# Performance work log

Hardware: AMD Instinct MI355X
Metric: run time of the kernel (lower is better)

## Reference

```python
import jax, jax.numpy as jnp
import numpy as np

H = 12
D_MODEL = 768
H_D = D_MODEL // H


def setup_inputs() -> dict:
    key = jax.random.key(0)
    ks = jax.random.split(key, 11)
    B, S = 2, 2048
    scale_in = 1.0
    w_scale = 1.0 / np.sqrt(D_MODEL)
    inp = {
        "query": jax.random.normal(ks[0], (B, S, D_MODEL), dtype=jnp.float32),
        "key": jax.random.normal(ks[1], (B, S, D_MODEL), dtype=jnp.float32),
        "value": jax.random.normal(ks[2], (B, S, D_MODEL), dtype=jnp.float32),
        "wq": jax.random.normal(ks[3], (D_MODEL, D_MODEL), dtype=jnp.float32) * w_scale,
        "bq": jnp.zeros((D_MODEL,), dtype=jnp.float32),
        "wk": jax.random.normal(ks[4], (D_MODEL, D_MODEL), dtype=jnp.float32) * w_scale,
        "bk": jnp.zeros((D_MODEL,), dtype=jnp.float32),
        "wv": jax.random.normal(ks[5], (D_MODEL, D_MODEL), dtype=jnp.float32) * w_scale,
        "bv": jnp.zeros((D_MODEL,), dtype=jnp.float32),
        "wo": jax.random.normal(ks[6], (D_MODEL, D_MODEL), dtype=jnp.float32) * w_scale,
        "bo": jnp.zeros((D_MODEL,), dtype=jnp.float32),
    }
    return inp


def reference(query, key, value, wq, bq, wk, bk, wv, bv, wo, bo):
    B, S, _ = query.shape
    # QKV projections, split into heads: [B, H, S, h_d]
    def proj(x, w, b):
        y = jnp.einsum("bsd,de->bse", x, w) + b
        return y.reshape(B, S, H, H_D).transpose(0, 2, 1, 3)

    q = proj(query, wq, bq)
    k = proj(key, wk, bk)
    v = proj(value, wv, bv)

    # scaled dot-product attention (dropout disabled / eval mode)
    scores = jnp.einsum("bhsd,bhtd->bhst", q, k) / jnp.sqrt(jnp.float32(H_D))
    wm = jax.nn.softmax(scores, axis=-1)  # [B, H, S, S]
    out = jnp.einsum("bhst,bhtd->bhsd", wm, v)

    # merge heads and output projection
    out = out.transpose(0, 2, 1, 3).reshape(B, S, D_MODEL)
    out = jnp.einsum("bsd,de->bse", out, wo) + bo
    return out
```

## Files before the change

kernel.cpp:

```cpp
#include <hip/hip_runtime.h>

#define H 12
#define DM 768
#define HD 64
#define SEQ 2048
#define BATCH 2
#define MROWS (BATCH*SEQ)

typedef __attribute__((ext_vector_type(8))) short short8;
typedef __attribute__((ext_vector_type(4))) float f32x4;
typedef __attribute__((ext_vector_type(16))) float f32x16;
using u16 = unsigned short;
using u32 = unsigned int;

__device__ __forceinline__ float bf2f(u16 u) { return __uint_as_float(((u32)u) << 16); }
__device__ __forceinline__ u16 f2bf(float x) {
  u32 u = __float_as_uint(x);
  return (u16)((u + 0x7fffu + ((u >> 16) & 1u)) >> 16);
}
__device__ __forceinline__ u32 cvt_pk_bf16(float lo, float hi) {
  u32 r;
  asm("v_cvt_pk_bf16_f32 %0, %1, %2" : "=v"(r) : "v"(lo), "v"(hi));
  return r;
}
__device__ __forceinline__ float fexp2(float x) {
  float r;
  asm("v_exp_f32 %0, %1" : "=v"(r) : "v"(x));
  return r;
}
__device__ __forceinline__ void gl2lds16(const u16* __restrict__ g, u16* l) {
  __builtin_amdgcn_global_load_lds(
      (const __attribute__((address_space(1))) unsigned int*)g,
      (__attribute__((address_space(3))) unsigned int*)l,
      16, 0, 0);
}

#define C_SM 0.18033688011112042f

__global__ __launch_bounds__(256) void transpose_w4(const float* __restrict__ w0, const float* __restrict__ w1,
                                                    const float* __restrict__ w2, const float* __restrict__ w3,
                                                    u16* __restrict__ dst0)
{
  __shared__ u16 Ts[64][72];
  const float* src = blockIdx.z == 0 ? w0 : blockIdx.z == 1 ? w1 : blockIdx.z == 2 ? w2 : w3;
  u16* dst = dst0 + (size_t)blockIdx.z * DM * DM;
  const int t = threadIdx.x;
  const int r0 = blockIdx.y * 64, c0 = blockIdx.x * 64;
  const int row = t >> 2, cq = (t & 3) * 16;
  const float* sp = src + (size_t)(r0 + row) * DM + c0 + cq;
  #pragma unroll
  for (int g = 0; g < 4; ++g) {
    float4 a = *reinterpret_cast<const float4*>(sp + g * 4);
    Ts[row][cq + g * 4 + 0] = f2bf(a.x);
    Ts[row][cq + g * 4 + 1] = f2bf(a.y);
    Ts[row][cq + g * 4 + 2] = f2bf(a.z);
    Ts[row][cq + g * 4 + 3] = f2bf(a.w);
  }
  __syncthreads();
  union { uint4 v[2]; u16 e[16]; } pk;
  #pragma unroll
  for (int j = 0; j < 16; ++j) pk.e[j] = Ts[cq + j][row];
  uint4* dp = reinterpret_cast<uint4*>(dst + (size_t)(c0 + row) * DM + r0 + cq);
  dp[0] = pk.v[0];
  dp[1] = pk.v[1];
}

template<int BM, bool AF32>
__device__ __forceinline__ void gemm_core(const void* __restrict__ Av, const u16* __restrict__ Bt,
                                          const float* __restrict__ bias, void* __restrict__ dstv,
                                          int mode, int bx, int by, float outScale)
{
  constexpr int AFR = BM / 32;
  constexpr int ACH = BM / 32;
  __shared__ u16 As[BM * 64];
  __shared__ u16 Bs[128 * 64];
  const int t = threadIdx.x;
  const int lane = t & 63, w = t >> 6;
  const int l15 = lane & 15, l4 = lane >> 4;
  const int m0 = by * BM, n0 = bx * 128;
  const int wr = (w >> 1) * (BM / 2), wc = (w & 1) * 64;

  f32x4 acc[AFR][4] = {};

  for (int kt = 0; kt < DM / 64; ++kt) {
    const int k0 = kt * 64;
    #pragma unroll
    for (int c = 0; c < ACH; ++c) {
      const int id = c * 256 + t;
      const int row = id >> 3, xc = id & 7;
      const int db = row * 128 + ((xc * 16) ^ ((row & 7) << 4));
      if (AF32) {
        const float* Af = reinterpret_cast<const float*>(Av) + (size_t)(m0 + row) * DM + k0 + xc * 8;
        float4 a0 = *reinterpret_cast<const float4*>(Af);
        float4 a1 = *reinterpret_cast<const float4*>(Af + 4);
        uint4 v;
        v.x = cvt_pk_bf16(a0.x, a0.y);
        v.y = cvt_pk_bf16(a0.z, a0.w);
        v.z = cvt_pk_bf16(a1.x, a1.y);
        v.w = cvt_pk_bf16(a1.z, a1.w);
        *reinterpret_cast<uint4*>(reinterpret_cast<char*>(As) + db) = v;
      } else {
        uint4 va = *reinterpret_cast<const uint4*>(reinterpret_cast<const u16*>(Av) +
                   (size_t)(m0 + row) * DM + k0 + xc * 8);
        *reinterpret_cast<uint4*>(reinterpret_cast<char*>(As) + db) = va;
      }
    }
    #pragma unroll
    for (int c = 0; c < 4; ++c) {
      const int id = c * 256 + t;
      const int row = id >> 3, xc = id & 7;
      const int db = row * 128 + ((xc * 16) ^ ((row & 7) << 4));
      uint4 vb = *reinterpret_cast<const uint4*>(Bt + (size_t)(n0 + row) * DM + k0 + xc * 8);
      *reinterpret_cast<uint4*>(reinterpret_cast<char*>(Bs) + db) = vb;
    }
    __syncthreads();
    #pragma unroll
    for (int ks = 0; ks < 2; ++ks) {
      short8 ag[AFR], bg[4];
      #pragma unroll
      for (int i = 0; i < AFR; ++i) {
        const int ar = wr + i * 16 + l15;
        ag[i] = *reinterpret_cast<const short8*>(reinterpret_cast<const char*>(As) +
                 ar * 128 + ((ks * 64 + l4 * 16) ^ ((ar & 7) << 4)));
      }
      #pragma unroll
      for (int j = 0; j < 4; ++j) {
        const int br = wc + j * 16 + l15;
        bg[j] = *reinterpret_cast<const short8*>(reinterpret_cast<const char*>(Bs) +
                 br * 128 + ((ks * 64 + l4 * 16) ^ ((br & 7) << 4)));
      }
      #pragma unroll
      for (int i = 0; i < AFR; ++i)
        #pragma unroll
        for (int j = 0; j < 4; ++j)
          acc[i][j] = __builtin_amdgcn_mfma_f32_16x16x32_bf16(ag[i], bg[j], acc[i][j], 0, 0, 0);
    }
    __syncthreads();
  }

  #pragma unroll
  for (int j = 0; j < 4; ++j) {
    const int gcol = n0 + wc + j * 16 + l15;
    const float bb = bias[gcol];
    #pragma unroll
    for (int i = 0; i < AFR; ++i) {
      const int grow = m0 + wr + i * 16 + l4 * 4;
      if (mode == 2) {
        float* dst = reinterpret_cast<float*>(dstv);
        #pragma unroll
        for (int r = 0; r < 4; ++r)
          dst[(size_t)(grow + r) * DM + gcol] = acc[i][j][r] + bb;
      } else {
        u16* dst = reinterpret_cast<u16*>(dstv);
        const int b = grow >> 11, s = grow & (SEQ - 1);
        const int h = gcol >> 6, d = gcol & 63;
        if (mode == 0) {
          #pragma unroll
          for (int r = 0; r < 4; ++r)
            dst[((size_t)(b * H + h) * SEQ + s + r) * HD + d] = f2bf((acc[i][j][r] + bb) * outScale);
        } else {
          union { uint2 v; u16 e[4]; } pk;
          #pragma unroll
          for (int r = 0; r < 4; ++r) pk.e[r] = f2bf(acc[i][j][r] + bb);
          *reinterpret_cast<uint2*>(dst + ((size_t)(b * H + h) * HD + d) * SEQ + s) = pk.v;
        }
      }
    }
  }
}

__global__ __launch_bounds__(256) void gemm_qkv_kernel(
    const float* __restrict__ xq, const float* __restrict__ xk, const float* __restrict__ xv,
    const u16* __restrict__ wT, const float* __restrict__ bq, const float* __restrict__ bk,
    const float* __restrict__ bv, u16* __restrict__ Qb, u16* __restrict__ Kb, u16* __restrict__ Vtb)
{
  const int flat = blockIdx.z * 384 + blockIdx.y * 6 + blockIdx.x;
  const int nb = (flat & 7) * 144 + (flat >> 3);
  const int z = nb / 384, rem = nb % 384;
  const int by = rem / 6, bx = rem % 6;
  const float* A    = z == 0 ? xq : z == 1 ? xk : xv;
  const u16* Bt     = wT + (size_t)z * DM * DM;
  const float* bias = z == 0 ? bq : z == 1 ? bk : bv;
  u16* dst          = z == 0 ? Qb : z == 1 ? Kb : Vtb;
  const float sc    = z == 1 ? C_SM : 1.0f;
  gemm_core<64, true>(A, Bt, bias, dst, z == 2 ? 1 : 0, bx, by, sc);
}

__global__ __launch_bounds__(256) void gemm_o_kernel(const u16* __restrict__ A, const u16* __restrict__ woT,
                                                     const float* __restrict__ bo, float* __restrict__ out)
{
  const int flat = blockIdx.y * 6 + blockIdx.x;
  const int nb = (flat & 7) * 96 + (flat >> 3);
  gemm_core<32, false>(A, woT, bo, out, 2, nb % 6, nb / 6, 1.0f);
}

__global__ __launch_bounds__(256) void attn_kernel(const u16* __restrict__ Q, const u16* __restrict__ K,
                                                   const u16* __restrict__ Vt,
                                                   float* __restrict__ Op0, float* __restrict__ Op1,
                                                   float* __restrict__ Lp0, float* __restrict__ Lp1)
{
  __shared__ u16 Ks[3][64 * 64];
  __shared__ u16 Vs[3][64 * 64];
  const int t = threadIdx.x;
  const int lane = t & 63, w = t >> 6;
  const int l31 = lane & 31, hi = lane >> 5;
  const int flat = blockIdx.y * 32 + blockIdx.x;
  const int nbid = (flat & 7) * 96 + (flat >> 3);
  const int bh = nbid >> 5;
  const int rem = nbid & 31;
  const int q0 = (rem >> 1) * 128;
  const int half = rem & 1;
  const int kv0 = half * (SEQ / 2);
  const size_t qbase  = ((size_t)bh * SEQ + q0) * HD;
  const size_t kbase0 = (size_t)bh * SEQ * HD;
  const size_t vtbase = (size_t)bh * HD * SEQ;
  float* __restrict__ Op = half ? Op1 : Op0;
  float* __restrict__ Lp = half ? Lp1 : Lp0;
  constexpr int NT = SEQ / 2 / 64;

  const int r8 = lane >> 3;
  const int pcol = ((lane & 7) ^ r8) * 8;

  short8 qf[4];
  {
    const u16* qp = Q + qbase + (size_t)(w * 32 + l31) * HD + hi * 8;
    #pragma unroll
    for (int ks = 0; ks < 4; ++ks)
      qf[ks] = *reinterpret_cast<const short8*>(qp + ks * 16);
  }

  auto STAGE = [&](int pt, int buf) {
    #pragma unroll
    for (int j = 0; j < 2; ++j) {
      const int ci = w * 2 + j;
      const int row = ci * 8 + r8;
      gl2lds16(K + kbase0 + (size_t)(kv0 + pt * 64 + row) * HD + pcol, &Ks[buf][ci * 512]);
      gl2lds16(Vt + vtbase + (size_t)row * SEQ + kv0 + pt * 64 + pcol, &Vs[buf][ci * 512]);
    }
  };

  STAGE(0, 0);
  STAGE(1, 1);

  short8 ones;
  #pragma unroll
  for (int j = 0; j < 8; ++j) ones[j] = (short)0x3F80;

  f32x16 oacc[2] = {};
  f32x16 accL = {};
  int cur = 0;

  for (int kt = 0; kt < NT; ++kt) {
    asm volatile("s_waitcnt vmcnt(4)" ::: "memory");
    __builtin_amdgcn_s_barrier();

    {
      const int pt = (kt + 2) & (NT - 1);
      const int pbuf = (cur + 2) % 3;
      STAGE(pt, pbuf);
    }

    f32x16 s0 = {}, s1 = {};
    __builtin_amdgcn_s_setprio(1);
    #pragma unroll
    for (int ks = 0; ks < 4; ++ks) {
      const int cb = ks * 32 + hi * 16;
      short8 kf0 = *reinterpret_cast<const short8*>(reinterpret_cast<const char*>(Ks[cur]) +
                   l31 * 128 + (cb ^ ((l31 & 7) << 4)));
      short8 kf1 = *reinterpret_cast<const short8*>(reinterpret_cast<const char*>(Ks[cur]) +
                   (32 + l31) * 128 + (cb ^ ((l31 & 7) << 4)));
      s0 = __builtin_amdgcn_mfma_f32_32x32x16_bf16(kf0, qf[ks], s0, 0, 0, 0);
      s1 = __builtin_amdgcn_mfma_f32_32x32x16_bf16(kf1, qf[ks], s1, 0, 0, 0);
    }
    __builtin_amdgcn_s_setprio(0);

    float p0[16], p1[16];
    #pragma unroll
    for (int r = 0; r < 16; ++r) {
      p0[r] = fexp2(s0[r]);
      p1[r] = fexp2(s1[r]);
    }

    __builtin_amdgcn_s_setprio(1);
    #pragma unroll
    for (int ks2 = 0; ks2 < 4; ++ks2) {
      const float* P = (ks2 < 2) ? p0 : p1;
      const int ro = (ks2 & 1) * 8;
      u32 a0 = cvt_pk_bf16(P[ro + 0], P[ro + 1]);
      u32 a1 = cvt_pk_bf16(P[ro + 2], P[ro + 3]);
      u32 b0 = cvt_pk_bf16(P[ro + 4], P[ro + 5]);
      u32 b1 = cvt_pk_bf16(P[ro + 6], P[ro + 7]);
      asm volatile("v_permlane32_swap_b32 %0, %1" : "+v"(a0), "+v"(b0));
      asm volatile("v_permlane32_swap_b32 %0, %1" : "+v"(a1), "+v"(b1));
      union { u32 u[4]; short8 s; } pa;
      pa.u[0] = a0; pa.u[1] = a1; pa.u[2] = b0; pa.u[3] = b1;
      accL = __builtin_amdgcn_mfma_f32_32x32x16_bf16(pa.s, ones, accL, 0, 0, 0);
      #pragma unroll
      for (int dt = 0; dt < 2; ++dt) {
        const int vr = dt * 32 + l31;
        short8 vf = *reinterpret_cast<const short8*>(reinterpret_cast<const char*>(Vs[cur]) +
                    vr * 128 + ((ks2 * 32 + hi * 16) ^ ((vr & 7) << 4)));
        oacc[dt] = __builtin_amdgcn_mfma_f32_32x32x16_bf16(pa.s, vf, oacc[dt], 0, 0, 0);
      }
    }
    __builtin_amdgcn_s_setprio(0);
    cur = (cur == 2) ? 0 : cur + 1;
  }

  if (l31 == 0) {
    #pragma unroll
    for (int r = 0; r < 16; ++r) {
      const int qo = (r & 3) + 8 * (r >> 2) + 4 * hi;
      Lp[(size_t)bh * SEQ + q0 + w * 32 + qo] = accL[r];
    }
  }
  #pragma unroll
  for (int r = 0; r < 16; ++r) {
    const int qo = (r & 3) + 8 * (r >> 2) + 4 * hi;
    const size_t base = ((size_t)bh * SEQ + q0 + w * 32 + qo) * HD;
    Op[base + l31]      = oacc[0][r];
    Op[base + 32 + l31] = oacc[1][r];
  }
}

__global__ __launch_bounds__(256) void attn_merge(const float* __restrict__ Op0, const float* __restrict__ Op1,
                                                  const float* __restrict__ Lp0, const float* __restrict__ Lp1,
                                                  u16* __restrict__ Ab)
{
  const int id = blockIdx.x * 256 + threadIdx.x;
  const int row = id >> 4, dc = (id & 15) * 4;
  const int bh = row >> 11, q = row & (SEQ - 1);
  const int b = bh / H, h = bh % H;
  const float inv = 1.f / (Lp0[row] + Lp1[row]);
  float4 o0 = *reinterpret_cast<const float4*>(Op0 + (size_t)row * HD + dc);
  float4 o1 = *reinterpret_cast<const float4*>(Op1 + (size_t)row * HD + dc);
  uint2 o;
  o.x = cvt_pk_bf16((o0.x + o1.x) * inv, (o0.y + o1.y) * inv);
  o.y = cvt_pk_bf16((o0.z + o1.z) * inv, (o0.w + o1.w) * inv);
  *reinterpret_cast<uint2*>(Ab + ((size_t)(b * SEQ + q)) * DM + h * HD + dc) = o;
}

extern "C" void kernel_launch(void* const* d_in, const int* in_sizes, int n_in,
                              void* d_out, int out_size, void* d_ws, size_t ws_size,
                              hipStream_t stream)
{
  const float* q  = (const float*)d_in[0];
  const float* k  = (const float*)d_in[1];
  const float* v  = (const float*)d_in[2];
  const float* wq = (const float*)d_in[3];
  const float* bq = (const float*)d_in[4];
  const float* wk = (const float*)d_in[5];
  const float* bk = (const float*)d_in[6];
  const float* wv = (const float*)d_in[7];
  const float* bv = (const float*)d_in[8];
  const float* wo = (const float*)d_in[9];
  const float* bo = (const float*)d_in[10];

  u16* ws = (u16*)d_ws;
  const size_t WSZ = (size_t)DM * DM;
  const size_t TSZ = (size_t)MROWS * DM;
  const size_t NQ  = (size_t)BATCH * H * SEQ;
  u16* wT  = ws;
  u16* Qb  = ws + 4 * WSZ;
  u16* Kb  = Qb + TSZ;
  u16* Vtb = Kb + TSZ;
  u16* Ab  = Vtb + TSZ;
  float* Op0 = (float*)(Ab + TSZ);
  float* Op1 = Op0 + TSZ;
  float* Lp0 = Op1 + TSZ;
  float* Lp1 = Lp0 + NQ;

  transpose_w4<<<dim3(12, 12, 4), 256, 0, stream>>>(wq, wk, wv, wo, wT);
  gemm_qkv_kernel<<<dim3(6, 64, 3), 256, 0, stream>>>(q, k, v, wT, bq, bk, bv, Qb, Kb, Vtb);
  attn_kernel<<<dim3(32, 24), 256, 0, stream>>>(Qb, Kb, Vtb, Op0, Op1, Lp0, Lp1);
  attn_merge<<<dim3((int)(NQ * 16 / 256)), 256, 0, stream>>>(Op0, Op1, Lp0, Lp1, Ab);
  gemm_o_kernel<<<dim3(6, 128), 256, 0, stream>>>(Ab, wT + 3 * WSZ, bo, (float*)d_out);
}
```

Baseline: 99.84 us.

## Pre-convert inputs to bf16 and triple-buffer GEMMs with async global-to-LDS loads

Adds a separate kernel that converts the fp32 q/k/v activations to bf16 into scratch space reused from the attention partial buffers. The projection GEMMs are rewritten around 64x64 tiles with a three-stage LDS ring filled by direct global-to-LDS loads, waited on with vmcnt and s_barrier, and given raised wave priority around the MFMA section. Grids double in the N dimension to match the smaller tiles. The aim is to hide global load latency behind compute and raise the number of blocks, at the cost of an extra pass over the inputs through memory and less register-level reuse per tile.

```diff
diff --git a/kernel.cpp b/kernel.cpp
--- a/kernel.cpp
+++ b/kernel.cpp
@@ -36,6 +36,27 @@
 }
 
 #define C_SM 0.18033688011112042f
+
+__global__ __launch_bounds__(256) void convert_x(const float* __restrict__ xq, const float* __restrict__ xk,
+                                                 const float* __restrict__ xv, u16* __restrict__ Xb)
+{
+  constexpr size_t N = (size_t)MROWS * DM;
+  constexpr size_t TOT = 3 * N / 8;
+  for (size_t id = (size_t)blockIdx.x * 256 + threadIdx.x; id < TOT; id += (size_t)gridDim.x * 256) {
+    const size_t e = id * 8;
+    const int z = (int)(e / N);
+    const size_t off = e - (size_t)z * N;
+    const float* src = z == 0 ? xq : z == 1 ? xk : xv;
+    float4 a0 = *reinterpret_cast<const float4*>(src + off);
+    float4 a1 = *reinterpret_cast<const float4*>(src + off + 4);
+    uint4 o;
+    o.x = cvt_pk_bf16(a0.x, a0.y);
+    o.y = cvt_pk_bf16(a0.z, a0.w);
+    o.z = cvt_pk_bf16(a1.x, a1.y);
+    o.w = cvt_pk_bf16(a1.z, a1.w);
+    *reinterpret_cast<uint4*>(Xb + (size_t)z * N + off) = o;
+  }
+}
 
 __global__ __launch_bounds__(256) void transpose_w4(const float* __restrict__ w0, const float* __restrict__ w1,
                                                     const float* __restrict__ w2, const float* __restrict__ w3,
@@ -65,85 +86,76 @@
   dp[1] = pk.v[1];
 }
 
-template<int BM, bool AF32>
-__device__ __forceinline__ void gemm_core(const void* __restrict__ Av, const u16* __restrict__ Bt,
+__device__ __forceinline__ void gemm_bf16(const u16* __restrict__ A, const u16* __restrict__ Bt,
                                           const float* __restrict__ bias, void* __restrict__ dstv,
                                           int mode, int bx, int by, float outScale)
 {
-  constexpr int AFR = BM / 32;
-  constexpr int ACH = BM / 32;
-  __shared__ u16 As[BM * 64];
-  __shared__ u16 Bs[128 * 64];
+  __shared__ u16 As[3][64 * 64];
+  __shared__ u16 Bs[3][64 * 64];
   const int t = threadIdx.x;
   const int lane = t & 63, w = t >> 6;
   const int l15 = lane & 15, l4 = lane >> 4;
-  const int m0 = by * BM, n0 = bx * 128;
-  const int wr = (w >> 1) * (BM / 2), wc = (w & 1) * 64;
-
-  f32x4 acc[AFR][4] = {};
-
-  for (int kt = 0; kt < DM / 64; ++kt) {
-    const int k0 = kt * 64;
-    #pragma unroll
-    for (int c = 0; c < ACH; ++c) {
-      const int id = c * 256 + t;
-      const int row = id >> 3, xc = id & 7;
-      const int db = row * 128 + ((xc * 16) ^ ((row & 7) << 4));
-      if (AF32) {
-        const float* Af = reinterpret_cast<const float*>(Av) + (size_t)(m0 + row) * DM + k0 + xc * 8;
-        float4 a0 = *reinterpret_cast<const float4*>(Af);
-        float4 a1 = *reinterpret_cast<const float4*>(Af + 4);
-        uint4 v;
-        v.x = cvt_pk_bf16(a0.x, a0.y);
-        v.y = cvt_pk_bf16(a0.z, a0.w);
-        v.z = cvt_pk_bf16(a1.x, a1.y);
-        v.w = cvt_pk_bf16(a1.z, a1.w);
-        *reinterpret_cast<uint4*>(reinterpret_cast<char*>(As) + db) = v;
-      } else {
-        uint4 va = *reinterpret_cast<const uint4*>(reinterpret_cast<const u16*>(Av) +
-                   (size_t)(m0 + row) * DM + k0 + xc * 8);
-        *reinterpret_cast<uint4*>(reinterpret_cast<char*>(As) + db) = va;
-      }
-    }
-    #pragma unroll
-    for (int c = 0; c < 4; ++c) {
-      const int id = c * 256 + t;
-      const int row = id >> 3, xc = id & 7;
-      const int db = row * 128 + ((xc * 16) ^ ((row & 7) << 4));
-      uint4 vb = *reinterpret_cast<const uint4*>(Bt + (size_t)(n0 + row) * DM + k0 + xc * 8);
-      *reinterpret_cast<uint4*>(reinterpret_cast<char*>(Bs) + db) = vb;
-    }
-    __syncthreads();
+  const int m0 = by * 64, n0 = bx * 64;
+  const int wr = (w >> 1) * 32, wc = (w & 1) * 32;
+  constexpr int NK = DM / 64;
+  const int r8 = lane >> 3;
+  const int pcol = ((lane & 7) ^ r8) * 8;
+
+  auto STAGE = [&](int kt2, int buf) {
+    const int k0 = kt2 * 64;
+    #pragma unroll
+    for (int j = 0; j < 2; ++j) {
+      const int ci = w * 2 + j;
+      const int row = ci * 8 + r8;
+      gl2lds16(A  + (size_t)(m0 + row) * DM + k0 + pcol, &As[buf][ci * 512]);
+      gl2lds16(Bt + (size_t)(n0 + row) * DM + k0 + pcol, &Bs[buf][ci * 512]);
+    }
+  };
+
+  STAGE(0, 0);
+  STAGE(1, 1);
+
+  f32x4 acc[2][2] = {};
+  int cur = 0;
+
+  for (int kt = 0; kt < NK; ++kt) {
+    asm volatile("s_waitcnt vmcnt(4)" ::: "memory");
+    __builtin_amdgcn_s_barrier();
+
+    {
+      int pt = kt + 2; if (pt >= NK) pt -= NK;
+      STAGE(pt, cur == 0 ? 2 : cur - 1);
+    }
+
+    __builtin_amdgcn_s_setprio(1);
     #pragma unroll
     for (int ks = 0; ks < 2; ++ks) {
-      short8 ag[AFR], bg[4];
+      short8 ag[2], bg[2];
       #pragma unroll
-      for (int i = 0; i < AFR; ++i) {
+      for (int i = 0; i < 2; ++i) {
         const int ar = wr + i * 16 + l15;
-        ag[i] = *reinterpret_cast<const short8*>(reinterpret_cast<const char*>(As) +
+        ag[i] = *reinterpret_cast<const short8*>(reinterpret_cast<const char*>(As[cur]) +
                  ar * 128 + ((ks * 64 + l4 * 16) ^ ((ar & 7) << 4)));
-      }
-      #pragma unroll
-      for (int j = 0; j < 4; ++j) {
-        const int br = wc + j * 16 + l15;
-        bg[j] = *reinterpret_cast<const short8*>(reinterpret_cast<const char*>(Bs) +
+        const int br = wc + i * 16 + l15;
+        bg[i] = *reinterpret_cast<const short8*>(reinterpret_cast<const char*>(Bs[cur]) +
                  br * 128 + ((ks * 64 + l4 * 16) ^ ((br & 7) << 4)));
       }
       #pragma unroll
-      for (int i = 0; i < AFR; ++i)
+      for (int i = 0; i < 2; ++i)
         #pragma unroll
-        for (int j = 0; j < 4; ++j)
+        for (int j = 0; j < 2; ++j)
           acc[i][j] = __builtin_amdgcn_mfma_f32_16x16x32_bf16(ag[i], bg[j], acc[i][j], 0, 0, 0);
     }
-    __syncthreads();
-  }
-
-  #pragma unroll
-  for (int j = 0; j < 4; ++j) {
+    __builtin_amdgcn_s_setprio(0);
+    cur = (cur == 2) ? 0 : cur + 1;
+  }
+
+  #pragma unroll
+  for (int j = 0; j < 2; ++j) {
     const int gcol = n0 + wc + j * 16 + l15;
     const float bb = bias[gcol];
     #pragma unroll
-    for (int i = 0; i < AFR; ++i) {
+    for (int i = 0; i < 2; ++i) {
       const int grow = m0 + wr + i * 16 + l4 * 4;
       if (mode == 2) {
         float* dst = reinterpret_cast<float*>(dstv);
@@ -170,28 +182,28 @@
 }
 
 __global__ __launch_bounds__(256) void gemm_qkv_kernel(
-    const float* __restrict__ xq, const float* __restrict__ xk, const float* __restrict__ xv,
-    const u16* __restrict__ wT, const float* __restrict__ bq, const float* __restrict__ bk,
-    const float* __restrict__ bv, u16* __restrict__ Qb, u16* __restrict__ Kb, u16* __restrict__ Vtb)
-{
-  const int flat = blockIdx.z * 384 + blockIdx.y * 6 + blockIdx.x;
-  const int nb = (flat & 7) * 144 + (flat >> 3);
-  const int z = nb / 384, rem = nb % 384;
-  const int by = rem / 6, bx = rem % 6;
-  const float* A    = z == 0 ? xq : z == 1 ? xk : xv;
+    const u16* __restrict__ Xb, const u16* __restrict__ wT,
+    const float* __restrict__ bq, const float* __restrict__ bk, const float* __restrict__ bv,
+    u16* __restrict__ Qb, u16* __restrict__ Kb, u16* __restrict__ Vtb)
+{
+  const int flat = blockIdx.z * 768 + blockIdx.y * 12 + blockIdx.x;
+  const int nb = (flat & 7) * 288 + (flat >> 3);
+  const int z = nb / 768, rem = nb % 768;
+  const int by = rem / 12, bx = rem % 12;
+  const u16* A      = Xb + (size_t)z * ((size_t)MROWS * DM);
   const u16* Bt     = wT + (size_t)z * DM * DM;
   const float* bias = z == 0 ? bq : z == 1 ? bk : bv;
   u16* dst          = z == 0 ? Qb : z == 1 ? Kb : Vtb;
   const float sc    = z == 1 ? C_SM : 1.0f;
-  gemm_core<64, true>(A, Bt, bias, dst, z == 2 ? 1 : 0, bx, by, sc);
+  gemm_bf16(A, Bt, bias, dst, z == 2 ? 1 : 0, bx, by, sc);
 }
 
 __global__ __launch_bounds__(256) void gemm_o_kernel(const u16* __restrict__ A, const u16* __restrict__ woT,
                                                      const float* __restrict__ bo, float* __restrict__ out)
 {
-  const int flat = blockIdx.y * 6 + blockIdx.x;
+  const int flat = blockIdx.y * 12 + blockIdx.x;
   const int nb = (flat & 7) * 96 + (flat >> 3);
-  gemm_core<32, false>(A, woT, bo, out, 2, nb % 6, nb / 6, 1.0f);
+  gemm_bf16(A, woT, bo, out, 2, nb % 12, nb / 12, 1.0f);
 }
 
 __global__ __launch_bounds__(256) void attn_kernel(const u16* __restrict__ Q, const u16* __restrict__ K,
@@ -369,10 +381,12 @@
   float* Op1 = Op0 + TSZ;
   float* Lp0 = Op1 + TSZ;
   float* Lp1 = Lp0 + NQ;
-
+  u16* Xb  = (u16*)Op0;
+
+  convert_x<<<dim3(2048), 256, 0, stream>>>(q, k, v, Xb);
   transpose_w4<<<dim3(12, 12, 4), 256, 0, stream>>>(wq, wk, wv, wo, wT);
-  gemm_qkv_kernel<<<dim3(6, 64, 3), 256, 0, stream>>>(q, k, v, wT, bq, bk, bv, Qb, Kb, Vtb);
+  gemm_qkv_kernel<<<dim3(12, 64, 3), 256, 0, stream>>>(Xb, wT, bq, bk, bv, Qb, Kb, Vtb);
   attn_kernel<<<dim3(32, 24), 256, 0, stream>>>(Qb, Kb, Vtb, Op0, Op1, Lp0, Lp1);
   attn_merge<<<dim3((int)(NQ * 16 / 256)), 256, 0, stream>>>(Op0, Op1, Lp0, Lp1, Ab);
-  gemm_o_kernel<<<dim3(6, 128), 256, 0, stream>>>(Ab, wT + 3 * WSZ, bo, (float*)d_out);
-}
+  gemm_o_kernel<<<dim3(12, 64), 256, 0, stream>>>(Ab, wT + 3 * WSZ, bo, (float*)d_out);
+}
```

Result: slower. 103.7 us (+3.9%).
